# Optimization experiments

Hardware: AMD Instinct MI355X
Metric: run time of the kernel (lower is better)

## Reference

```python
import jax, jax.numpy as jnp
import numpy as np

EPS = 1e-8  # torch F.cosine_similarity norm clamp


def setup_inputs() -> dict:
    key = jax.random.key(0)
    k1, k2, k3, k4 = jax.random.split(key, 4)
    B, N, M, D, T = 8, 4096, 2048, 512, 2
    return {
        "features": jax.random.normal(k1, (B, N, D), dtype=jnp.float32),
        "text": jax.random.normal(k2, (T, M, D), dtype=jnp.float32),
        "W": jax.random.normal(k3, (D, D), dtype=jnp.float32) * 0.02,
        "b": jax.random.normal(k4, (D,), dtype=jnp.float32) * 0.02,
    }


def reference(features, text, W, b):
    # features: [B, N, D] (output of the extractor), text: [T, M, D]
    B, N, D = features.shape
    f1 = jnp.einsum("bnd,de->bne", features, W) + b  # linear_layer(features)
    t1 = text[1]  # [M, D]; expanded across batch (row 1 per original code)

    # cosine similarity over last dim without materializing [B, N, M, D]
    fn = f1 / jnp.maximum(jnp.linalg.norm(f1, axis=-1, keepdims=True), EPS)
    tn = t1 / jnp.maximum(jnp.linalg.norm(t1, axis=-1, keepdims=True), EPS)
    sim = jnp.einsum("bnd,md->bnm", fn, tn)  # [B, N, M]

    e = jnp.exp(sim)
    w = e / jnp.sum(e, axis=1, keepdims=True)  # normalize over N (dim=1)

    # features_t [B,D,N] @ w [B,N,M] -> [B,D,M] -> transpose -> [B,M,D]
    fm = jnp.einsum("bnd,bnm->bmd", features, w)

    t1b = jnp.broadcast_to(t1[None, :, :], (B,) + t1.shape)  # [B, M, D]
    combine_feature = jnp.concatenate([fm, t1b], axis=2)  # [B, M, 2D]
    return combine_feature
```

## Files before the change

### kernel.cpp

```cpp
#include <hip/hip_runtime.h>

#define B_SZ 8
#define N_SZ 4096
#define M_SZ 2048
#define D_SZ 512

typedef __attribute__((ext_vector_type(8))) short bf16x8;
typedef __attribute__((ext_vector_type(4))) float f32x4;
typedef __attribute__((address_space(1))) const void* gptr1;
typedef __attribute__((address_space(3))) void* lptr3;

__device__ __forceinline__ unsigned short f2bf(float x) {
    unsigned int u = __builtin_bit_cast(unsigned int, x);
    u += 0x7fffu + ((u >> 16) & 1u);
    return (unsigned short)(u >> 16);
}
__device__ __forceinline__ float bf2f(unsigned short u) {
    unsigned int x = ((unsigned int)u) << 16;
    return __builtin_bit_cast(float, x);
}

__device__ __forceinline__ void bt_mainloop(
    const unsigned short* __restrict__ A, const unsigned short* __restrict__ Bt,
    int lda, int ldb, int rowBase, int colBase, int K,
    unsigned short* As, unsigned short* Bs, f32x4 acc[4][4])
{
    const int tid  = threadIdx.x;
    const int lane = tid & 63;
    const int w    = tid >> 6;
    const int wr   = (w >> 1) * 64;
    const int wc   = (w & 1) * 64;
    const int lr   = lane & 15;
    const int kq   = lane >> 4;

    const int srow0 = w * 16 + (lane >> 2);
    const int skk   = (lane & 3) * 8;

    for (int k0 = 0; k0 < K; k0 += 32) {
#pragma unroll
        for (int j = 0; j < 2; ++j) {
            const unsigned short* ga = A  + (size_t)(rowBase + srow0 + j * 64) * lda + (k0 + skk);
            const unsigned short* gb = Bt + (size_t)(colBase + srow0 + j * 64) * ldb + (k0 + skk);
            __builtin_amdgcn_global_load_lds((gptr1)ga, (lptr3)(As + (j * 4 + w) * 512), 16, 0, 0);
            __builtin_amdgcn_global_load_lds((gptr1)gb, (lptr3)(Bs + (j * 4 + w) * 512), 16, 0, 0);
        }
        asm volatile("s_waitcnt vmcnt(0)" ::: "memory");
        __syncthreads();

        bf16x8 af[4], bq[4];
#pragma unroll
        for (int i = 0; i < 4; ++i) {
            af[i] = *(const bf16x8*)(As + (wr + i * 16 + lr) * 32 + kq * 8);
            bq[i] = *(const bf16x8*)(Bs + (wc + i * 16 + lr) * 32 + kq * 8);
        }
#pragma unroll
        for (int mi = 0; mi < 4; ++mi)
#pragma unroll
            for (int ni = 0; ni < 4; ++ni)
                acc[mi][ni] = __builtin_amdgcn_mfma_f32_16x16x32_bf16(af[mi], bq[ni], acc[mi][ni], 0, 0, 0);
        __syncthreads();
    }
}

__global__ __launch_bounds__(256) void prep_tn_k(
    const float* __restrict__ text, unsigned short* __restrict__ tn,
    float* __restrict__ out, float* __restrict__ L, float* __restrict__ SS)
{
    const int m = blockIdx.x;
    const int t = threadIdx.x;
    const float* t1 = text + (size_t)M_SZ * D_SZ;
    float2 v = ((const float2*)(t1 + (size_t)m * D_SZ))[t];
    float s = v.x * v.x + v.y * v.y;
#pragma unroll
    for (int off = 32; off > 0; off >>= 1) s += __shfl_down(s, off);
    __shared__ float partial[4];
    if ((t & 63) == 0) partial[t >> 6] = s;
    __syncthreads();
    float norm = sqrtf(partial[0] + partial[1] + partial[2] + partial[3]);
    norm = fmaxf(norm, 1e-8f);
    const float inv = 1.f / norm;
    ushort2 pk; pk.x = f2bf(v.x * inv); pk.y = f2bf(v.y * inv);
    ((ushort2*)(tn + (size_t)m * D_SZ))[t] = pk;
#pragma unroll
    for (int b = 0; b < B_SZ; ++b)
        ((float2*)(out + ((size_t)(b * M_SZ + m)) * (2 * D_SZ) + D_SZ))[t] = v;
    if (m < 64) L[m * 256 + t] = 0.f;
    if (m < 128) SS[m * 256 + t] = 0.f;
}

__global__ __launch_bounds__(256) void prep_w_k(
    const float* __restrict__ W, unsigned short* __restrict__ Wt)
{
    const int dt = blockIdx.x, et = blockIdx.y;
    const int t = threadIdx.x;
    __shared__ unsigned short tile[64][72];
    const int rr = t >> 4;
    const int cc = (t & 15) * 4;
#pragma unroll
    for (int p = 0; p < 4; ++p) {
        const int d = p * 16 + rr;
        const float4 v = *(const float4*)(W + (size_t)(dt * 64 + d) * D_SZ + et * 64 + cc);
        tile[d][cc] = f2bf(v.x); tile[d][cc + 1] = f2bf(v.y);
        tile[d][cc + 2] = f2bf(v.z); tile[d][cc + 3] = f2bf(v.w);
    }
    __syncthreads();
#pragma unroll
    for (int p = 0; p < 4; ++p) {
        const int e = p * 16 + rr;
        ushort4 pk;
        pk.x = tile[cc][e]; pk.y = tile[cc + 1][e]; pk.z = tile[cc + 2][e]; pk.w = tile[cc + 3][e];
        *(ushort4*)(Wt + (size_t)(et * 64 + e) * D_SZ + dt * 64 + cc) = pk;
    }
}

__global__ __launch_bounds__(256) void convert_feat_k(
    const float* __restrict__ feat, unsigned short* __restrict__ V,
    unsigned short* __restrict__ Vt)
{
    const int nt = blockIdx.x, dt = blockIdx.y, b = blockIdx.z;
    const int t = threadIdx.x;
    __shared__ unsigned short tile[64][72];
    const int rr = t >> 4;
    const int cc = (t & 15) * 4;
#pragma unroll
    for (int p = 0; p < 4; ++p) {
        const int r = p * 16 + rr;
        const size_t grow = (size_t)(b * N_SZ + nt * 64 + r);
        const float4 v = *(const float4*)(feat + grow * D_SZ + dt * 64 + cc);
        ushort4 pk; pk.x = f2bf(v.x); pk.y = f2bf(v.y); pk.z = f2bf(v.z); pk.w = f2bf(v.w);
        *(ushort4*)(V + grow * D_SZ + dt * 64 + cc) = pk;
        tile[r][cc] = pk.x; tile[r][cc + 1] = pk.y; tile[r][cc + 2] = pk.z; tile[r][cc + 3] = pk.w;
    }
    __syncthreads();
#pragma unroll
    for (int p = 0; p < 4; ++p) {
        const int d = p * 16 + rr;
        ushort4 pk;
        pk.x = tile[cc][d]; pk.y = tile[cc + 1][d]; pk.z = tile[cc + 2][d]; pk.w = tile[cc + 3][d];
        *(ushort4*)(Vt + ((size_t)(b * D_SZ + dt * 64 + d)) * N_SZ + nt * 64 + cc) = pk;
    }
}

__global__ __launch_bounds__(256) void gemm1_k(
    const unsigned short* __restrict__ V, const unsigned short* __restrict__ Wt,
    const float* __restrict__ bias, unsigned short* __restrict__ f1b,
    float* __restrict__ SS)
{
    __shared__ unsigned short As[128 * 32];
    __shared__ unsigned short Bs[128 * 32];
    f32x4 acc[4][4];
#pragma unroll
    for (int i = 0; i < 4; ++i)
#pragma unroll
        for (int j = 0; j < 4; ++j) acc[i][j] = (f32x4){0.f, 0.f, 0.f, 0.f};
    const int tid = threadIdx.x, lane = tid & 63, w = tid >> 6;
    const int wr = (w >> 1) * 64, wc = (w & 1) * 64, lr = lane & 15, kq = lane >> 4;

    const int rowBase = blockIdx.x * 128;
    const int colBase = blockIdx.y * 128;
    bt_mainloop(V, Wt, D_SZ, D_SZ, rowBase, colBase, D_SZ, As, Bs, acc);

#pragma unroll
    for (int mi = 0; mi < 4; ++mi) {
        const int r0 = rowBase + wr + mi * 16 + kq * 4;
        float s[4] = {0.f, 0.f, 0.f, 0.f};
#pragma unroll
        for (int ni = 0; ni < 4; ++ni) {
            const int c = colBase + wc + ni * 16 + lr;
            const float bv = bias[c];
#pragma unroll
            for (int r = 0; r < 4; ++r) {
                const float v = acc[mi][ni][r] + bv;
                f1b[(size_t)(r0 + r) * D_SZ + c] = f2bf(v);
                s[r] += v * v;
            }
        }
#pragma unroll
        for (int off = 1; off <= 8; off <<= 1)
#pragma unroll
            for (int r = 0; r < 4; ++r) s[r] += __shfl_xor(s[r], off);
        if (lr == 0) {
#pragma unroll
            for (int r = 0; r < 4; ++r) atomicAdd(&SS[r0 + r], s[r]);
        }
    }
}

__global__ __launch_bounds__(128) void normalize_k(
    const unsigned short* __restrict__ f1b, const float* __restrict__ SS,
    unsigned short* __restrict__ fn)
{
    const int row = blockIdx.x;
    const int t = threadIdx.x;
    const float norm = fmaxf(sqrtf(SS[row]), 1e-8f);
    const float inv = 1.f / norm;
    ushort4 v = ((const ushort4*)(f1b + (size_t)row * D_SZ))[t];
    ushort4 o;
    o.x = f2bf(bf2f(v.x) * inv); o.y = f2bf(bf2f(v.y) * inv);
    o.z = f2bf(bf2f(v.z) * inv); o.w = f2bf(bf2f(v.w) * inv);
    ((ushort4*)(fn + (size_t)row * D_SZ))[t] = o;
}

__global__ __launch_bounds__(256) void gemm2_k(
    const unsigned short* __restrict__ fn, const unsigned short* __restrict__ tn,
    unsigned short* __restrict__ E, float* __restrict__ L)
{
    __shared__ unsigned short smem[128 * 136];
    unsigned short* As = smem;
    unsigned short* Bs = smem + 4096;
    f32x4 acc[4][4];
#pragma unroll
    for (int i = 0; i < 4; ++i)
#pragma unroll
        for (int j = 0; j < 4; ++j) acc[i][j] = (f32x4){0.f, 0.f, 0.f, 0.f};
    const int tid = threadIdx.x, lane = tid & 63, w = tid >> 6;
    const int wr = (w >> 1) * 64, wc = (w & 1) * 64, lr = lane & 15, kq = lane >> 4;

    const int lin = blockIdx.x;
    const int xcd = lin & 7, slot = lin >> 3;
    const int mt = slot & 15;
    const int rt = (slot >> 4) * 8 + xcd;
    const int rowBase = rt * 128;
    const int colBase = mt * 128;

    bt_mainloop(fn, tn, D_SZ, D_SZ, rowBase, colBase, D_SZ, As, Bs, acc);

    const int b  = rowBase >> 12;
    const int nb = rowBase & 4095;
    unsigned short* Eb = E + (size_t)b * M_SZ * N_SZ;
    unsigned short* P = smem;

#pragma unroll
    for (int ni = 0; ni < 4; ++ni) {
        const int mm = wc + ni * 16 + lr;
        float p = 0.f;
#pragma unroll
        for (int mi = 0; mi < 4; ++mi) {
            const int nn0 = wr + mi * 16 + kq * 4;
            const float e0 = __expf(acc[mi][ni][0]);
            const float e1 = __expf(acc[mi][ni][1]);
            const float e2 = __expf(acc[mi][ni][2]);
            const float e3 = __expf(acc[mi][ni][3]);
            ushort4 pk; pk.x = f2bf(e0); pk.y = f2bf(e1); pk.z = f2bf(e2); pk.w = f2bf(e3);
            *(ushort4*)(P + mm * 136 + nn0) = pk;
            p += (e0 + e1) + (e2 + e3);
        }
        p += __shfl_down(p, 16);
        p += __shfl_down(p, 32);
        if (lane < 16) atomicAdd(&L[b * M_SZ + colBase + mm], p);
    }
    __syncthreads();

    const int tr = tid >> 4;
    const int tc = (tid & 15) * 8;
#pragma unroll
    for (int j = 0; j < 8; ++j) {
        const int mm = j * 16 + tr;
        bf16x8 v = *(const bf16x8*)(P + mm * 136 + tc);
        *(bf16x8*)(Eb + (size_t)(colBase + mm) * N_SZ + nb + tc) = v;
    }
}

__global__ __launch_bounds__(256) void gemm3_k(
    const unsigned short* __restrict__ E, const unsigned short* __restrict__ Vt,
    const float* __restrict__ L, float* __restrict__ out)
{
    __shared__ unsigned short As[128 * 32];
    __shared__ unsigned short Bs[128 * 32];
    f32x4 acc[4][4];
#pragma unroll
    for (int i = 0; i < 4; ++i)
#pragma unroll
        for (int j = 0; j < 4; ++j) acc[i][j] = (f32x4){0.f, 0.f, 0.f, 0.f};
    const int tid = threadIdx.x, lane = tid & 63, w = tid >> 6;
    const int wr = (w >> 1) * 64, wc = (w & 1) * 64, lr = lane & 15, kq = lane >> 4;

    const int b = blockIdx.z;
    const int rowBase = blockIdx.x * 128;
    const int colBase = blockIdx.y * 128;
    const unsigned short* Ab = E + (size_t)b * M_SZ * N_SZ;
    const unsigned short* Bb = Vt + (size_t)b * D_SZ * N_SZ;
    bt_mainloop(Ab, Bb, N_SZ, N_SZ, rowBase, colBase, N_SZ, As, Bs, acc);

#pragma unroll
    for (int mi = 0; mi < 4; ++mi) {
        const int r0 = rowBase + wr + mi * 16 + kq * 4;
        float invl[4];
#pragma unroll
        for (int r = 0; r < 4; ++r) invl[r] = 1.f / L[b * M_SZ + r0 + r];
#pragma unroll
        for (int ni = 0; ni < 4; ++ni) {
            const int d = colBase + wc + ni * 16 + lr;
#pragma unroll
            for (int r = 0; r < 4; ++r)
                out[((size_t)(b * M_SZ + r0 + r)) * (2 * D_SZ) + d] = acc[mi][ni][r] * invl[r];
        }
    }
}

extern "C" void kernel_launch(void* const* d_in, const int* in_sizes, int n_in,
                              void* d_out, int out_size, void* d_ws, size_t ws_size,
                              hipStream_t stream) {
    const float* features = (const float*)d_in[0];
    const float* text     = (const float*)d_in[1];
    const float* W        = (const float*)d_in[2];
    const float* bias     = (const float*)d_in[3];
    float* out = (float*)d_out;
    char* ws = (char*)d_ws;

    unsigned short* fn  = (unsigned short*)(ws + 0);
    unsigned short* tn  = (unsigned short*)(ws + 33554432);
    unsigned short* Wt  = (unsigned short*)(ws + 35651584);
    unsigned short* V   = (unsigned short*)(ws + 36175872);
    unsigned short* Vt  = (unsigned short*)(ws + 69730304);
    float*          L   = (float*)(ws + 103284736);
    float*          SS  = (float*)(ws + 103350272);
    unsigned short* E   = (unsigned short*)(ws + 103481344);
    unsigned short* f1b = (unsigned short*)(ws + 103481344);

    hipLaunchKernelGGL(prep_tn_k, dim3(M_SZ), dim3(256), 0, stream, text, tn, out, L, SS);
    hipLaunchKernelGGL(prep_w_k, dim3(8, 8), dim3(256), 0, stream, W, Wt);
    hipLaunchKernelGGL(convert_feat_k, dim3(64, 8, 8), dim3(256), 0, stream, features, V, Vt);
    hipLaunchKernelGGL(gemm1_k, dim3(256, 4), dim3(256), 0, stream, V, Wt, bias, f1b, SS);
    hipLaunchKernelGGL(normalize_k, dim3(32768), dim3(128), 0, stream, f1b, SS, fn);
    hipLaunchKernelGGL(gemm2_k, dim3(4096), dim3(256), 0, stream, fn, tn, E, L);
    hipLaunchKernelGGL(gemm3_k, dim3(16, 4, 8), dim3(256), 0, stream, E, Vt, L, out);
}
```

Baseline: 383.5 us.

## Reassociate linear layer into text side and split-K the final GEMM

The similarity is rewritten algebraically as features·(W·t) plus b·t, scaled by per-row and per-column inverse norms. This removes the f1 materialization and the separate normalize kernel, and gemm2 now consumes the raw bf16 features with a precomputed W·t1 matrix. Gemm1 only computes row sums of squares, plus a small extra GEMM for W·t. Gemm3 splits K in two with atomic accumulation into a zeroed output, which doubles the block count. The costs are atomic float adds on the output and a different bf16 rounding path for the similarity.

Measured after the change: 419.6 us. 1.09x slower.

```diff
diff --git a/kernel.cpp b/kernel.cpp
--- a/kernel.cpp
+++ b/kernel.cpp
@@ -14,10 +14,6 @@
     unsigned int u = __builtin_bit_cast(unsigned int, x);
     u += 0x7fffu + ((u >> 16) & 1u);
     return (unsigned short)(u >> 16);
-}
-__device__ __forceinline__ float bf2f(unsigned short u) {
-    unsigned int x = ((unsigned int)u) << 16;
-    return __builtin_bit_cast(float, x);
 }
 
 __device__ __forceinline__ void bt_mainloop(
@@ -62,34 +58,42 @@
     }
 }
 
-__global__ __launch_bounds__(256) void prep_tn_k(
-    const float* __restrict__ text, unsigned short* __restrict__ tn,
+__global__ __launch_bounds__(256) void prep_t_k(
+    const float* __restrict__ text, const float* __restrict__ bias,
+    unsigned short* __restrict__ t1bf, float* __restrict__ invs, float* __restrict__ c2,
     float* __restrict__ out, float* __restrict__ L, float* __restrict__ SS)
 {
     const int m = blockIdx.x;
     const int t = threadIdx.x;
     const float* t1 = text + (size_t)M_SZ * D_SZ;
     float2 v = ((const float2*)(t1 + (size_t)m * D_SZ))[t];
+    float2 bb = ((const float2*)bias)[t];
     float s = v.x * v.x + v.y * v.y;
-#pragma unroll
-    for (int off = 32; off > 0; off >>= 1) s += __shfl_down(s, off);
-    __shared__ float partial[4];
-    if ((t & 63) == 0) partial[t >> 6] = s;
+    float c = v.x * bb.x + v.y * bb.y;
+#pragma unroll
+    for (int off = 32; off > 0; off >>= 1) { s += __shfl_down(s, off); c += __shfl_down(c, off); }
+    __shared__ float ps[4], pc[4];
+    if ((t & 63) == 0) { ps[t >> 6] = s; pc[t >> 6] = c; }
     __syncthreads();
-    float norm = sqrtf(partial[0] + partial[1] + partial[2] + partial[3]);
-    norm = fmaxf(norm, 1e-8f);
-    const float inv = 1.f / norm;
-    ushort2 pk; pk.x = f2bf(v.x * inv); pk.y = f2bf(v.y * inv);
-    ((ushort2*)(tn + (size_t)m * D_SZ))[t] = pk;
-#pragma unroll
-    for (int b = 0; b < B_SZ; ++b)
+    if (t == 0) {
+        float norm = fmaxf(sqrtf(ps[0] + ps[1] + ps[2] + ps[3]), 1e-8f);
+        invs[m] = 1.f / norm;
+        c2[m] = pc[0] + pc[1] + pc[2] + pc[3];
+    }
+    ushort2 pk; pk.x = f2bf(v.x); pk.y = f2bf(v.y);
+    ((ushort2*)(t1bf + (size_t)m * D_SZ))[t] = pk;
+#pragma unroll
+    for (int b = 0; b < B_SZ; ++b) {
         ((float2*)(out + ((size_t)(b * M_SZ + m)) * (2 * D_SZ) + D_SZ))[t] = v;
+        ((float2*)(out + ((size_t)(b * M_SZ + m)) * (2 * D_SZ)))[t] = (float2){0.f, 0.f};
+    }
     if (m < 64) L[m * 256 + t] = 0.f;
     if (m < 128) SS[m * 256 + t] = 0.f;
 }
 
 __global__ __launch_bounds__(256) void prep_w_k(
-    const float* __restrict__ W, unsigned short* __restrict__ Wt)
+    const float* __restrict__ W, unsigned short* __restrict__ Wt,
+    unsigned short* __restrict__ Wbf)
 {
     const int dt = blockIdx.x, et = blockIdx.y;
     const int t = threadIdx.x;
@@ -100,8 +104,9 @@
     for (int p = 0; p < 4; ++p) {
         const int d = p * 16 + rr;
         const float4 v = *(const float4*)(W + (size_t)(dt * 64 + d) * D_SZ + et * 64 + cc);
-        tile[d][cc] = f2bf(v.x); tile[d][cc + 1] = f2bf(v.y);
-        tile[d][cc + 2] = f2bf(v.z); tile[d][cc + 3] = f2bf(v.w);
+        ushort4 pk; pk.x = f2bf(v.x); pk.y = f2bf(v.y); pk.z = f2bf(v.z); pk.w = f2bf(v.w);
+        *(ushort4*)(Wbf + (size_t)(dt * 64 + d) * D_SZ + et * 64 + cc) = pk;
+        tile[d][cc] = pk.x; tile[d][cc + 1] = pk.y; tile[d][cc + 2] = pk.z; tile[d][cc + 3] = pk.w;
     }
     __syncthreads();
 #pragma unroll
@@ -141,10 +146,11 @@
     }
 }
 
-__global__ __launch_bounds__(256) void gemm1_k(
+__global__ __launch_bounds__(256) void gemm1f_k(
     const unsigned short* __restrict__ V, const unsigned short* __restrict__ Wt,
-    const float* __restrict__ bias, unsigned short* __restrict__ f1b,
-    float* __restrict__ SS)
+    const float* __restrict__ bias, float* __restrict__ SS,
+    const unsigned short* __restrict__ t1bf, const unsigned short* __restrict__ Wbf,
+    unsigned short* __restrict__ ttn)
 {
     __shared__ unsigned short As[128 * 32];
     __shared__ unsigned short Bs[128 * 32];
@@ -155,55 +161,59 @@
         for (int j = 0; j < 4; ++j) acc[i][j] = (f32x4){0.f, 0.f, 0.f, 0.f};
     const int tid = threadIdx.x, lane = tid & 63, w = tid >> 6;
     const int wr = (w >> 1) * 64, wc = (w & 1) * 64, lr = lane & 15, kq = lane >> 4;
-
-    const int rowBase = blockIdx.x * 128;
-    const int colBase = blockIdx.y * 128;
-    bt_mainloop(V, Wt, D_SZ, D_SZ, rowBase, colBase, D_SZ, As, Bs, acc);
-
-#pragma unroll
-    for (int mi = 0; mi < 4; ++mi) {
-        const int r0 = rowBase + wr + mi * 16 + kq * 4;
-        float s[4] = {0.f, 0.f, 0.f, 0.f};
-#pragma unroll
-        for (int ni = 0; ni < 4; ++ni) {
-            const int c = colBase + wc + ni * 16 + lr;
-            const float bv = bias[c];
-#pragma unroll
-            for (int r = 0; r < 4; ++r) {
-                const float v = acc[mi][ni][r] + bv;
-                f1b[(size_t)(r0 + r) * D_SZ + c] = f2bf(v);
-                s[r] += v * v;
+    const int blk = blockIdx.x;
+
+    if (blk < 64) {
+        const int rowBase = (blk >> 2) * 128;
+        const int colBase = (blk & 3) * 128;
+        bt_mainloop(t1bf, Wbf, D_SZ, D_SZ, rowBase, colBase, D_SZ, As, Bs, acc);
+#pragma unroll
+        for (int mi = 0; mi < 4; ++mi) {
+            const int r0 = rowBase + wr + mi * 16 + kq * 4;
+#pragma unroll
+            for (int ni = 0; ni < 4; ++ni) {
+                const int c = colBase + wc + ni * 16 + lr;
+#pragma unroll
+                for (int r = 0; r < 4; ++r)
+                    ttn[(size_t)(r0 + r) * D_SZ + c] = f2bf(acc[mi][ni][r]);
             }
         }
-#pragma unroll
-        for (int off = 1; off <= 8; off <<= 1)
-#pragma unroll
-            for (int r = 0; r < 4; ++r) s[r] += __shfl_xor(s[r], off);
-        if (lr == 0) {
-#pragma unroll
-            for (int r = 0; r < 4; ++r) atomicAdd(&SS[r0 + r], s[r]);
-        }
-    }
-}
-
-__global__ __launch_bounds__(128) void normalize_k(
-    const unsigned short* __restrict__ f1b, const float* __restrict__ SS,
-    unsigned short* __restrict__ fn)
-{
-    const int row = blockIdx.x;
-    const int t = threadIdx.x;
-    const float norm = fmaxf(sqrtf(SS[row]), 1e-8f);
-    const float inv = 1.f / norm;
-    ushort4 v = ((const ushort4*)(f1b + (size_t)row * D_SZ))[t];
-    ushort4 o;
-    o.x = f2bf(bf2f(v.x) * inv); o.y = f2bf(bf2f(v.y) * inv);
-    o.z = f2bf(bf2f(v.z) * inv); o.w = f2bf(bf2f(v.w) * inv);
-    ((ushort4*)(fn + (size_t)row * D_SZ))[t] = o;
+    } else {
+        const int bb = blk - 64;
+        const int rowBase = (bb >> 2) * 128;
+        const int colBase = (bb & 3) * 128;
+        bt_mainloop(V, Wt, D_SZ, D_SZ, rowBase, colBase, D_SZ, As, Bs, acc);
+#pragma unroll
+        for (int mi = 0; mi < 4; ++mi) {
+            const int r0 = rowBase + wr + mi * 16 + kq * 4;
+            float s[4] = {0.f, 0.f, 0.f, 0.f};
+#pragma unroll
+            for (int ni = 0; ni < 4; ++ni) {
+                const int c = colBase + wc + ni * 16 + lr;
+                const float bv = bias[c];
+#pragma unroll
+                for (int r = 0; r < 4; ++r) {
+                    const float v = acc[mi][ni][r] + bv;
+                    s[r] += v * v;
+                }
+            }
+#pragma unroll
+            for (int off = 1; off <= 8; off <<= 1)
+#pragma unroll
+                for (int r = 0; r < 4; ++r) s[r] += __shfl_xor(s[r], off);
+            if (lr == 0) {
+#pragma unroll
+                for (int r = 0; r < 4; ++r) atomicAdd(&SS[r0 + r], s[r]);
+            }
+        }
+    }
 }
 
 __global__ __launch_bounds__(256) void gemm2_k(
-    const unsigned short* __restrict__ fn, const unsigned short* __restrict__ tn,
-    unsigned short* __restrict__ E, float* __restrict__ L)
+    const unsigned short* __restrict__ V, const unsigned short* __restrict__ ttn,
+    const float* __restrict__ SS, const float* __restrict__ invs,
+    const float* __restrict__ c2, unsigned short* __restrict__ E,
+    float* __restrict__ L)
 {
     __shared__ unsigned short smem[128 * 136];
     unsigned short* As = smem;
@@ -223,24 +233,35 @@
     const int rowBase = rt * 128;
     const int colBase = mt * 128;
 
-    bt_mainloop(fn, tn, D_SZ, D_SZ, rowBase, colBase, D_SZ, As, Bs, acc);
+    bt_mainloop(V, ttn, D_SZ, D_SZ, rowBase, colBase, D_SZ, As, Bs, acc);
 
     const int b  = rowBase >> 12;
     const int nb = rowBase & 4095;
     unsigned short* Eb = E + (size_t)b * M_SZ * N_SZ;
     unsigned short* P = smem;
 
+    float invr[4][4];
+#pragma unroll
+    for (int mi = 0; mi < 4; ++mi) {
+        const int r0 = rowBase + wr + mi * 16 + kq * 4;
+#pragma unroll
+        for (int r = 0; r < 4; ++r)
+            invr[mi][r] = 1.f / fmaxf(sqrtf(SS[r0 + r]), 1e-8f);
+    }
+
 #pragma unroll
     for (int ni = 0; ni < 4; ++ni) {
         const int mm = wc + ni * 16 + lr;
+        const float sm = invs[colBase + mm];
+        const float cm = c2[colBase + mm];
         float p = 0.f;
 #pragma unroll
         for (int mi = 0; mi < 4; ++mi) {
             const int nn0 = wr + mi * 16 + kq * 4;
-            const float e0 = __expf(acc[mi][ni][0]);
-            const float e1 = __expf(acc[mi][ni][1]);
-            const float e2 = __expf(acc[mi][ni][2]);
-            const float e3 = __expf(acc[mi][ni][3]);
+            const float e0 = __expf((acc[mi][ni][0] + cm) * invr[mi][0] * sm);
+            const float e1 = __expf((acc[mi][ni][1] + cm) * invr[mi][1] * sm);
+            const float e2 = __expf((acc[mi][ni][2] + cm) * invr[mi][2] * sm);
+            const float e3 = __expf((acc[mi][ni][3] + cm) * invr[mi][3] * sm);
             ushort4 pk; pk.x = f2bf(e0); pk.y = f2bf(e1); pk.z = f2bf(e2); pk.w = f2bf(e3);
             *(ushort4*)(P + mm * 136 + nn0) = pk;
             p += (e0 + e1) + (e2 + e3);
@@ -275,12 +296,18 @@
     const int tid = threadIdx.x, lane = tid & 63, w = tid >> 6;
     const int wr = (w >> 1) * 64, wc = (w & 1) * 64, lr = lane & 15, kq = lane >> 4;
 
-    const int b = blockIdx.z;
-    const int rowBase = blockIdx.x * 128;
-    const int colBase = blockIdx.y * 128;
-    const unsigned short* Ab = E + (size_t)b * M_SZ * N_SZ;
-    const unsigned short* Bb = Vt + (size_t)b * D_SZ * N_SZ;
-    bt_mainloop(Ab, Bb, N_SZ, N_SZ, rowBase, colBase, N_SZ, As, Bs, acc);
+    const int lin = blockIdx.x;
+    const int dt = lin >> 8;
+    const int g  = lin & 255;
+    const int b  = g >> 5;
+    const int mt = (g & 31) >> 1;
+    const int kh = g & 1;
+
+    const int rowBase = mt * 128;
+    const int colBase = dt * 128;
+    const unsigned short* Ab = E  + (size_t)b * M_SZ * N_SZ + (size_t)kh * 2048;
+    const unsigned short* Bb = Vt + (size_t)b * D_SZ * N_SZ + (size_t)kh * 2048;
+    bt_mainloop(Ab, Bb, N_SZ, N_SZ, rowBase, colBase, 2048, As, Bs, acc);
 
 #pragma unroll
     for (int mi = 0; mi < 4; ++mi) {
@@ -293,7 +320,8 @@
             const int d = colBase + wc + ni * 16 + lr;
 #pragma unroll
             for (int r = 0; r < 4; ++r)
-                out[((size_t)(b * M_SZ + r0 + r)) * (2 * D_SZ) + d] = acc[mi][ni][r] * invl[r];
+                atomicAdd(&out[((size_t)(b * M_SZ + r0 + r)) * (2 * D_SZ) + d],
+                          acc[mi][ni][r] * invl[r]);
         }
     }
 }
@@ -308,21 +336,25 @@
     float* out = (float*)d_out;
     char* ws = (char*)d_ws;
 
-    unsigned short* fn  = (unsigned short*)(ws + 0);
-    unsigned short* tn  = (unsigned short*)(ws + 33554432);
-    unsigned short* Wt  = (unsigned short*)(ws + 35651584);
-    unsigned short* V   = (unsigned short*)(ws + 36175872);
-    unsigned short* Vt  = (unsigned short*)(ws + 69730304);
-    float*          L   = (float*)(ws + 103284736);
-    float*          SS  = (float*)(ws + 103350272);
-    unsigned short* E   = (unsigned short*)(ws + 103481344);
-    unsigned short* f1b = (unsigned short*)(ws + 103481344);
-
-    hipLaunchKernelGGL(prep_tn_k, dim3(M_SZ), dim3(256), 0, stream, text, tn, out, L, SS);
-    hipLaunchKernelGGL(prep_w_k, dim3(8, 8), dim3(256), 0, stream, W, Wt);
+    unsigned short* t1bf = (unsigned short*)(ws + 0);
+    unsigned short* ttn  = (unsigned short*)(ws + 2097152);
+    unsigned short* Wt   = (unsigned short*)(ws + 4194304);
+    unsigned short* Wbf  = (unsigned short*)(ws + 4718592);
+    unsigned short* V    = (unsigned short*)(ws + 5242880);
+    unsigned short* Vt   = (unsigned short*)(ws + 38797312);
+    float*          L    = (float*)(ws + 72351744);
+    float*          SS   = (float*)(ws + 72417280);
+    float*          invs = (float*)(ws + 72548352);
+    float*          c2   = (float*)(ws + 72556544);
+    unsigned short* E    = (unsigned short*)(ws + 72564736);
+
+    hipLaunchKernelGGL(prep_t_k, dim3(M_SZ), dim3(256), 0, stream,
+                       text, bias, t1bf, invs, c2, out, L, SS);
+    hipLaunchKernelGGL(prep_w_k, dim3(8, 8), dim3(256), 0, stream, W, Wt, Wbf);
     hipLaunchKernelGGL(convert_feat_k, dim3(64, 8, 8), dim3(256), 0, stream, features, V, Vt);
-    hipLaunchKernelGGL(gemm1_k, dim3(256, 4), dim3(256), 0, stream, V, Wt, bias, f1b, SS);
-    hipLaunchKernelGGL(normalize_k, dim3(32768), dim3(128), 0, stream, f1b, SS, fn);
-    hipLaunchKernelGGL(gemm2_k, dim3(4096), dim3(256), 0, stream, fn, tn, E, L);
-    hipLaunchKernelGGL(gemm3_k, dim3(16, 4, 8), dim3(256), 0, stream, E, Vt, L, out);
-}
+    hipLaunchKernelGGL(gemm1f_k, dim3(1088), dim3(256), 0, stream,
+                       V, Wt, bias, SS, t1bf, Wbf, ttn);
+    hipLaunchKernelGGL(gemm2_k, dim3(4096), dim3(256), 0, stream,
+                       V, ttn, SS, invs, c2, E, L);
+    hipLaunchKernelGGL(gemm3_k, dim3(1024), dim3(256), 0, stream, E, Vt, L, out);
+}
```
